# Kernel optimization log

Measured on AMD Instinct MI355X. Metric: run time of the kernel, lower is better.

Reference implementation:

```python
import jax, jax.numpy as jnp
import numpy as np

N, L, H, M, D = 4096, 4096, 8, 64, 64

def setup_inputs() -> dict:
    key = jax.random.key(0)
    kq, kk, kv = jax.random.split(key, 3)
    queries = jax.random.normal(kq, (N, H, M), dtype=jnp.float32)
    keys = jax.random.normal(kk, (L, H, M), dtype=jnp.float32)
    values = jax.random.normal(kv, (L, H, D), dtype=jnp.float32)
    return {"queries": queries, "keys": keys, "values": values}

def reference(queries, keys, values):
    # scores: [n, l, h] = sigmoid(q . k) per head
    attention_num = jax.nn.sigmoid(jnp.einsum('nhm,lhm->nlh', queries, keys))
    # normalizer: sum over l -> [n, h] (torch code broadcasts via wasteful repeat)
    attention_normalizer = jnp.sum(attention_num, axis=1, keepdims=True)  # [n,1,h]
    attention = attention_num / attention_normalizer  # [n,l,h]
    # dropout p=0.0 -> identity
    attn_output = jnp.einsum('nlh,lhd->nhd', attention, values)
    return attn_output
```

## Files before the change

kernel.cpp:

```cpp
#include <hip/hip_runtime.h>
#include <stdint.h>


typedef __bf16 bf16x8 __attribute__((ext_vector_type(8)));
typedef __bf16 bf16x2 __attribute__((ext_vector_type(2)));
typedef float  f32x2  __attribute__((ext_vector_type(2)));
typedef float  f32x16 __attribute__((ext_vector_type(16)));

constexpr int NH = 8, MD = 64, NL = 4096, NN = 4096;
constexpr size_t ONUM_ELEMS = (size_t)NN * NH * MD;
constexpr size_t Z_ELEMS    = (size_t)NN * NH;
constexpr size_t KB_ELEMS   = (size_t)NH * NL * MD;
constexpr size_t VTB_ELEMS  = (size_t)NH * NL * MD;

__device__ __forceinline__ unsigned packbf2(float a, float b) {
  bf16x2 t = __builtin_convertvector((f32x2){a, b}, bf16x2);
  return __builtin_bit_cast(unsigned, t);
}

__device__ __forceinline__ void glds16(const void* g, void* l) {
  __builtin_amdgcn_global_load_lds(
      (const __attribute__((address_space(1))) unsigned int*)g,
      (__attribute__((address_space(3))) unsigned int*)l, 16, 0, 0);
}

__global__ __launch_bounds__(256) void diffattn_prepass(
    const float* __restrict__ Kg, const float* __restrict__ Vg,
    unsigned short* __restrict__ Kb, unsigned short* __restrict__ Vtb) {
  __shared__ __attribute__((aligned(16))) unsigned short Vt_lds[64 * 64];
  const int tid = threadIdx.x;
  const int h = blockIdx.x & 7;
  const int t = blockIdx.x >> 3;

#pragma unroll
  for (int e = 0; e < 2; ++e) {
    const int g = tid * 2 + e;
    const int l = g >> 3, c = g & 7;
    const float* kp = Kg + (((size_t)(t * 64 + l) * NH + h) * MD) + c * 8;
    const float4 a = *(const float4*)kp;
    const float4 b = *(const float4*)(kp + 4);
    unsigned out[4] = {packbf2(a.x, a.y), packbf2(a.z, a.w),
                       packbf2(b.x, b.y), packbf2(b.z, b.w)};
    unsigned short* dst =
        Kb + ((size_t)h * NL + t * 64 + l) * MD + ((c ^ (l & 7)) * 8);
    *(uint4*)dst = *(const uint4*)out;
  }

  {
    const int lr = tid & 63, dbase = (tid >> 6) * 16;
    const float* vp = Vg + (((size_t)(t * 64 + lr) * NH + h) * MD) + dbase;
#pragma unroll
    for (int i = 0; i < 4; ++i) {
      const float4 v = *(const float4*)(vp + i * 4);
      const int d0 = dbase + i * 4;
      Vt_lds[(d0 + 0) * 64 + lr] = __builtin_bit_cast(unsigned short, (__bf16)v.x);
      Vt_lds[(d0 + 1) * 64 + lr] = __builtin_bit_cast(unsigned short, (__bf16)v.y);
      Vt_lds[(d0 + 2) * 64 + lr] = __builtin_bit_cast(unsigned short, (__bf16)v.z);
      Vt_lds[(d0 + 3) * 64 + lr] = __builtin_bit_cast(unsigned short, (__bf16)v.w);
    }
  }
  __syncthreads();
#pragma unroll
  for (int e = 0; e < 2; ++e) {
    const int g = tid * 2 + e;
    const int d = g >> 3, cl = g & 7;
    const uint4 chunk = *(const uint4*)&Vt_lds[d * 64 + cl * 8];
    unsigned short* dst = Vtb + ((size_t)(h * 64 + t) * 64 + d) * 64 +
                          ((cl ^ (d & 7)) * 8);
    *(uint4*)dst = chunk;
  }
}

__global__ __launch_bounds__(256, 4) void diffattn_partial(
    const float* __restrict__ Qg, const unsigned short* __restrict__ Kb,
    const unsigned short* __restrict__ Vtb, float* __restrict__ Onum,
    float* __restrict__ Zp, int nsplit, int lLen) {
  __shared__ __attribute__((aligned(16))) unsigned short Ksh[64 * 64];
  __shared__ __attribute__((aligned(16))) unsigned short Vtsh[64 * 64];

  const int tid  = threadIdx.x;
  const int w    = tid >> 6;
  const int lane = tid & 63;
  const int col  = lane & 31;
  const int hi   = lane >> 5;

  const int h     = blockIdx.x & 7;
  const int tmp   = blockIdx.x >> 3;
  const int split = tmp % nsplit;
  const int n0    = (tmp / nsplit) * 128;
  const int lBeg  = split * lLen;

  bf16x8 qf[4];
  {
    const float* qp = Qg + ((size_t)(n0 + w * 32 + col) * NH + h) * MD;
    const float c = -1.4426950408889634f;
#pragma unroll
    for (int kc = 0; kc < 4; ++kc) {
      const float4 x = *(const float4*)(qp + kc * 16 + hi * 8);
      const float4 y = *(const float4*)(qp + kc * 16 + hi * 8 + 4);
      bf16x8 f;
      f[0] = (__bf16)(c * x.x); f[1] = (__bf16)(c * x.y);
      f[2] = (__bf16)(c * x.z); f[3] = (__bf16)(c * x.w);
      f[4] = (__bf16)(c * y.x); f[5] = (__bf16)(c * y.y);
      f[6] = (__bf16)(c * y.z); f[7] = (__bf16)(c * y.w);
      qf[kc] = f;
    }
  }

  f32x16 oacc[2];
#pragma unroll
  for (int i = 0; i < 16; ++i) { oacc[0][i] = 0.f; oacc[1][i] = 0.f; }
  float zacc = 0.f;

  const char* kgh = (const char*)(Kb + (size_t)h * NL * MD);
  const char* vgh = (const char*)(Vtb + (size_t)h * NL * MD);

  for (int l0 = lBeg; l0 < lBeg + lLen; l0 += 64) {
    const char* kgb = kgh + (size_t)l0 * 128;
    const char* vgb = vgh + (size_t)l0 * 128;
    __syncthreads();
    {
      const int o = w * 2048 + lane * 16;
      glds16(kgb + o,        (char*)Ksh  + w * 2048);
      glds16(kgb + o + 1024, (char*)Ksh  + w * 2048 + 1024);
      glds16(vgb + o,        (char*)Vtsh + w * 2048);
      glds16(vgb + o + 1024, (char*)Vtsh + w * 2048 + 1024);
    }
    __syncthreads();

    f32x16 d1[2];
#pragma unroll
    for (int i = 0; i < 16; ++i) { d1[0][i] = 0.f; d1[1][i] = 0.f; }
#pragma unroll
    for (int lh = 0; lh < 2; ++lh) {
      const int rowK = lh * 32 + col;
      const char* kp = (const char*)Ksh + rowK * 128;
      const int sw = rowK & 7;
#pragma unroll
      for (int kc = 0; kc < 4; ++kc) {
        const bf16x8 kf = *(const bf16x8*)(kp + (((kc << 1) | hi) ^ sw) * 16);
        d1[lh] = __builtin_amdgcn_mfma_f32_32x32x16_bf16(kf, qf[kc], d1[lh], 0, 0, 0);
      }
    }

    unsigned pk[2][8];
#pragma unroll
    for (int lh = 0; lh < 2; ++lh) {
      float s[16];
#pragma unroll
      for (int r = 0; r < 16; ++r) {
        const float e = __builtin_amdgcn_exp2f(d1[lh][r]);
        s[r] = __builtin_amdgcn_rcpf(1.0f + e);
        zacc += s[r];
      }
#pragma unroll
      for (int p = 0; p < 8; ++p) pk[lh][p] = packbf2(s[2 * p], s[2 * p + 1]);
    }

#pragma unroll
    for (int kc2 = 0; kc2 < 4; ++kc2) {
      const int lh = kc2 >> 1, s4 = (kc2 & 1) * 4;
      const unsigned send0 = hi ? pk[lh][s4 + 0] : pk[lh][s4 + 2];
      const unsigned send1 = hi ? pk[lh][s4 + 1] : pk[lh][s4 + 3];
      const unsigned recv0 = (unsigned)__shfl_xor((int)send0, 32, 64);
      const unsigned recv1 = (unsigned)__shfl_xor((int)send1, 32, 64);
      union { unsigned u[4]; bf16x8 v; } pf;
      if (hi == 0) {
        pf.u[0] = pk[lh][s4 + 0]; pf.u[1] = pk[lh][s4 + 1];
        pf.u[2] = recv0;          pf.u[3] = recv1;
      } else {
        pf.u[0] = recv0;          pf.u[1] = recv1;
        pf.u[2] = pk[lh][s4 + 2]; pf.u[3] = pk[lh][s4 + 3];
      }
#pragma unroll
      for (int ds = 0; ds < 2; ++ds) {
        const int rowV = ds * 32 + col;
        const bf16x8 vf = *(const bf16x8*)((const char*)Vtsh + rowV * 128 +
                                           (((kc2 << 1) | hi) ^ (rowV & 7)) * 16);
        oacc[ds] = __builtin_amdgcn_mfma_f32_32x32x16_bf16(pf.v, vf, oacc[ds], 0, 0, 0);
      }
    }
  }

  const float zrow = zacc + __shfl_xor(zacc, 32, 64);
  if (hi == 0)
    Zp[(size_t)split * Z_ELEMS + (size_t)(n0 + w * 32 + col) * NH + h] = zrow;

  float* onum = Onum + (size_t)split * ONUM_ELEMS;
#pragma unroll
  for (int ds = 0; ds < 2; ++ds) {
    const int d = ds * 32 + col;
#pragma unroll
    for (int r = 0; r < 16; ++r) {
      const int row = (r & 3) + 8 * (r >> 2) + 4 * hi;
      onum[((size_t)(n0 + w * 32 + row) * NH + h) * MD + d] = oacc[ds][r];
    }
  }
}

__global__ __launch_bounds__(256) void diffattn_combine(
    const float* __restrict__ Onum, const float* __restrict__ Zp,
    float* __restrict__ Og, int nsplit) {
  const int idx = blockIdx.x * 256 + threadIdx.x;
  if (idx >= (int)(ONUM_ELEMS / 4)) return;
  const int nh = idx >> 4;
  const int d4 = (idx & 15) * 4;
  float z = 0.f;
  float4 o = make_float4(0.f, 0.f, 0.f, 0.f);
  for (int s = 0; s < nsplit; ++s) {
    z += Zp[(size_t)s * Z_ELEMS + nh];
    const float4 t = *(const float4*)(Onum + (size_t)s * ONUM_ELEMS +
                                      (size_t)nh * MD + d4);
    o.x += t.x; o.y += t.y; o.z += t.z; o.w += t.w;
  }
  const float zi = __builtin_amdgcn_rcpf(z);
  float4 r = make_float4(o.x * zi, o.y * zi, o.z * zi, o.w * zi);
  *(float4*)(Og + (size_t)nh * MD + d4) = r;
}

extern "C" void kernel_launch(void* const* d_in, const int* in_sizes, int n_in,
                              void* d_out, int out_size, void* d_ws, size_t ws_size,
                              hipStream_t stream) {
  const float* Q = (const float*)d_in[0];
  const float* K = (const float*)d_in[1];
  const float* V = (const float*)d_in[2];
  float* O = (float*)d_out;

  const size_t conv_bytes = (KB_ELEMS + VTB_ELEMS) * sizeof(unsigned short);
  int nsplit = 4;
  while (nsplit > 1 &&
         (size_t)nsplit * (ONUM_ELEMS + Z_ELEMS) * sizeof(float) + conv_bytes >
             ws_size)
    nsplit >>= 1;

  float* Onum = (float*)d_ws;
  float* Zp   = Onum + (size_t)nsplit * ONUM_ELEMS;
  unsigned short* Kbb = (unsigned short*)(Zp + (size_t)nsplit * Z_ELEMS);
  unsigned short* Vtb = Kbb + KB_ELEMS;

  const int lLen = NL / nsplit;
  diffattn_prepass<<<dim3(8 * (NL / 64)), dim3(256), 0, stream>>>(K, V, Kbb, Vtb);
  diffattn_partial<<<dim3(8 * 32 * nsplit), dim3(256), 0, stream>>>(
      Q, Kbb, Vtb, Onum, Zp, nsplit, lLen);
  diffattn_combine<<<dim3((ONUM_ELEMS / 4 + 255) / 256), dim3(256), 0, stream>>>(
      Onum, Zp, O, nsplit);
}
```

Before: 131.6 us.

## Fuse split-L combine into partial kernel via atomic last-block reduction

Drops the separate combine kernel. Each partial block now increments a per-(n-tile, head) atomic counter, and the last block to finish sums the split partial numerators and normalizers and writes the final output. The split count also rises from 4 to 8 to put more blocks on the GPU. The intent is to save a kernel launch and improve occupancy. In exchange it adds a memset, fences, and a serialized tail reduction in the last block, plus twice the partial-buffer traffic.

```diff
diff --git a/kernel.cpp b/kernel.cpp
--- a/kernel.cpp
+++ b/kernel.cpp
@@ -12,6 +12,7 @@
 constexpr size_t Z_ELEMS    = (size_t)NN * NH;
 constexpr size_t KB_ELEMS   = (size_t)NH * NL * MD;
 constexpr size_t VTB_ELEMS  = (size_t)NH * NL * MD;
+constexpr int NGROUPS = 8 * 32;
 
 __device__ __forceinline__ unsigned packbf2(float a, float b) {
   bf16x2 t = __builtin_convertvector((f32x2){a, b}, bf16x2);
@@ -74,9 +75,12 @@
 __global__ __launch_bounds__(256, 4) void diffattn_partial(
     const float* __restrict__ Qg, const unsigned short* __restrict__ Kb,
     const unsigned short* __restrict__ Vtb, float* __restrict__ Onum,
-    float* __restrict__ Zp, int nsplit, int lLen) {
+    float* __restrict__ Zp, int* __restrict__ cnt, float* __restrict__ Og,
+    int nsplit, int lLen) {
   __shared__ __attribute__((aligned(16))) unsigned short Ksh[64 * 64];
   __shared__ __attribute__((aligned(16))) unsigned short Vtsh[64 * 64];
+  __shared__ float Zred[128];
+  __shared__ int lastSh;
 
   const int tid  = threadIdx.x;
   const int w    = tid >> 6;
@@ -87,7 +91,8 @@
   const int h     = blockIdx.x & 7;
   const int tmp   = blockIdx.x >> 3;
   const int split = tmp % nsplit;
-  const int n0    = (tmp / nsplit) * 128;
+  const int ntile = tmp / nsplit;
+  const int n0    = ntile * 128;
   const int lBeg  = split * lLen;
 
   bf16x8 qf[4];
@@ -196,26 +201,36 @@
       onum[((size_t)(n0 + w * 32 + row) * NH + h) * MD + d] = oacc[ds][r];
     }
   }
-}
-
-__global__ __launch_bounds__(256) void diffattn_combine(
-    const float* __restrict__ Onum, const float* __restrict__ Zp,
-    float* __restrict__ Og, int nsplit) {
-  const int idx = blockIdx.x * 256 + threadIdx.x;
-  if (idx >= (int)(ONUM_ELEMS / 4)) return;
-  const int nh = idx >> 4;
-  const int d4 = (idx & 15) * 4;
-  float z = 0.f;
-  float4 o = make_float4(0.f, 0.f, 0.f, 0.f);
-  for (int s = 0; s < nsplit; ++s) {
-    z += Zp[(size_t)s * Z_ELEMS + nh];
-    const float4 t = *(const float4*)(Onum + (size_t)s * ONUM_ELEMS +
-                                      (size_t)nh * MD + d4);
-    o.x += t.x; o.y += t.y; o.z += t.z; o.w += t.w;
-  }
-  const float zi = __builtin_amdgcn_rcpf(z);
-  float4 r = make_float4(o.x * zi, o.y * zi, o.z * zi, o.w * zi);
-  *(float4*)(Og + (size_t)nh * MD + d4) = r;
+
+  __threadfence();
+  __syncthreads();
+  if (tid == 0) {
+    const int gid = ntile * 8 + h;
+    lastSh = (atomicAdd(&cnt[gid], 1) == nsplit - 1) ? 1 : 0;
+  }
+  __syncthreads();
+  if (!lastSh) return;
+
+  __threadfence();
+  for (int r = tid; r < 128; r += 256) {
+    float z = 0.f;
+    for (int s = 0; s < nsplit; ++s)
+      z += Zp[(size_t)s * Z_ELEMS + (size_t)(n0 + r) * NH + h];
+    Zred[r] = __builtin_amdgcn_rcpf(z);
+  }
+  __syncthreads();
+  for (int j = tid; j < 128 * 16; j += 256) {
+    const int r = j >> 4, c4 = j & 15;
+    const size_t off = ((size_t)(n0 + r) * NH + h) * MD + c4 * 4;
+    float4 acc = make_float4(0.f, 0.f, 0.f, 0.f);
+    for (int s = 0; s < nsplit; ++s) {
+      const float4 t = *(const float4*)(Onum + (size_t)s * ONUM_ELEMS + off);
+      acc.x += t.x; acc.y += t.y; acc.z += t.z; acc.w += t.w;
+    }
+    const float zi = Zred[r];
+    *(float4*)(Og + off) =
+        make_float4(acc.x * zi, acc.y * zi, acc.z * zi, acc.w * zi);
+  }
 }
 
 extern "C" void kernel_launch(void* const* d_in, const int* in_sizes, int n_in,
@@ -226,8 +241,9 @@
   const float* V = (const float*)d_in[2];
   float* O = (float*)d_out;
 
-  const size_t conv_bytes = (KB_ELEMS + VTB_ELEMS) * sizeof(unsigned short);
-  int nsplit = 4;
+  const size_t conv_bytes =
+      (KB_ELEMS + VTB_ELEMS) * sizeof(unsigned short) + NGROUPS * sizeof(int);
+  int nsplit = 8;
   while (nsplit > 1 &&
          (size_t)nsplit * (ONUM_ELEMS + Z_ELEMS) * sizeof(float) + conv_bytes >
              ws_size)
@@ -237,11 +253,11 @@
   float* Zp   = Onum + (size_t)nsplit * ONUM_ELEMS;
   unsigned short* Kbb = (unsigned short*)(Zp + (size_t)nsplit * Z_ELEMS);
   unsigned short* Vtb = Kbb + KB_ELEMS;
-
+  int* cnt = (int*)(Vtb + VTB_ELEMS);
+
+  hipMemsetAsync(cnt, 0, NGROUPS * sizeof(int), stream);
   const int lLen = NL / nsplit;
   diffattn_prepass<<<dim3(8 * (NL / 64)), dim3(256), 0, stream>>>(K, V, Kbb, Vtb);
   diffattn_partial<<<dim3(8 * 32 * nsplit), dim3(256), 0, stream>>>(
-      Q, Kbb, Vtb, Onum, Zp, nsplit, lLen);
-  diffattn_combine<<<dim3((ONUM_ELEMS / 4 + 255) / 256), dim3(256), 0, stream>>>(
-      Onum, Zp, O, nsplit);
-}
+      Q, Kbb, Vtb, Onum, Zp, cnt, O, nsplit, lLen);
+}
```

Result: slower. 441.1 us (+235.2%).

## Double-buffer K/V tiles in LDS to prefetch the next tile during compute

Applied to the files above, without the earlier changes.

The K and V^T tiles in shared memory become two ping-pong buffers. The async global-to-LDS load of tile t+1 is issued right after the barrier, then tile t is computed, leaving one barrier per iteration instead of two. The goal is to hide global-load latency behind the MFMA and sigmoid work. The first MFMA of the score chain now takes a constant zero accumulator instead of zeroing registers. The cost is twice the LDS per block, which could limit how many blocks fit on a CU.

```diff
diff --git a/kernel.cpp b/kernel.cpp
--- a/kernel.cpp
+++ b/kernel.cpp
@@ -75,8 +75,8 @@
     const float* __restrict__ Qg, const unsigned short* __restrict__ Kb,
     const unsigned short* __restrict__ Vtb, float* __restrict__ Onum,
     float* __restrict__ Zp, int nsplit, int lLen) {
-  __shared__ __attribute__((aligned(16))) unsigned short Ksh[64 * 64];
-  __shared__ __attribute__((aligned(16))) unsigned short Vtsh[64 * 64];
+  __shared__ __attribute__((aligned(16))) unsigned short Ksh[2][64 * 64];
+  __shared__ __attribute__((aligned(16))) unsigned short Vtsh[2][64 * 64];
 
   const int tid  = threadIdx.x;
   const int w    = tid >> 6;
@@ -111,33 +111,46 @@
 #pragma unroll
   for (int i = 0; i < 16; ++i) { oacc[0][i] = 0.f; oacc[1][i] = 0.f; }
   float zacc = 0.f;
+  const f32x16 zf = {};
 
   const char* kgh = (const char*)(Kb + (size_t)h * NL * MD);
   const char* vgh = (const char*)(Vtb + (size_t)h * NL * MD);
-
-  for (int l0 = lBeg; l0 < lBeg + lLen; l0 += 64) {
-    const char* kgb = kgh + (size_t)l0 * 128;
-    const char* vgb = vgh + (size_t)l0 * 128;
+  const int o = w * 2048 + lane * 16;
+  const int T = lLen >> 6;
+
+  {
+    const char* kgb = kgh + (size_t)lBeg * 128;
+    const char* vgb = vgh + (size_t)lBeg * 128;
+    glds16(kgb + o,        (char*)Ksh[0]  + w * 2048);
+    glds16(kgb + o + 1024, (char*)Ksh[0]  + w * 2048 + 1024);
+    glds16(vgb + o,        (char*)Vtsh[0] + w * 2048);
+    glds16(vgb + o + 1024, (char*)Vtsh[0] + w * 2048 + 1024);
+  }
+
+  for (int t = 0; t < T; ++t) {
+    const int cur = t & 1;
     __syncthreads();
-    {
-      const int o = w * 2048 + lane * 16;
-      glds16(kgb + o,        (char*)Ksh  + w * 2048);
-      glds16(kgb + o + 1024, (char*)Ksh  + w * 2048 + 1024);
-      glds16(vgb + o,        (char*)Vtsh + w * 2048);
-      glds16(vgb + o + 1024, (char*)Vtsh + w * 2048 + 1024);
-    }
-    __syncthreads();
+    if (t + 1 < T) {
+      const char* kgb = kgh + (size_t)(lBeg + (t + 1) * 64) * 128;
+      const char* vgb = vgh + (size_t)(lBeg + (t + 1) * 64) * 128;
+      glds16(kgb + o,        (char*)Ksh[cur ^ 1]  + w * 2048);
+      glds16(kgb + o + 1024, (char*)Ksh[cur ^ 1]  + w * 2048 + 1024);
+      glds16(vgb + o,        (char*)Vtsh[cur ^ 1] + w * 2048);
+      glds16(vgb + o + 1024, (char*)Vtsh[cur ^ 1] + w * 2048 + 1024);
+    }
 
     f32x16 d1[2];
-#pragma unroll
-    for (int i = 0; i < 16; ++i) { d1[0][i] = 0.f; d1[1][i] = 0.f; }
 #pragma unroll
     for (int lh = 0; lh < 2; ++lh) {
       const int rowK = lh * 32 + col;
-      const char* kp = (const char*)Ksh + rowK * 128;
+      const char* kp = (const char*)Ksh[cur] + rowK * 128;
       const int sw = rowK & 7;
-#pragma unroll
-      for (int kc = 0; kc < 4; ++kc) {
+      {
+        const bf16x8 kf = *(const bf16x8*)(kp + ((hi ^ sw) * 16));
+        d1[lh] = __builtin_amdgcn_mfma_f32_32x32x16_bf16(kf, qf[0], zf, 0, 0, 0);
+      }
+#pragma unroll
+      for (int kc = 1; kc < 4; ++kc) {
         const bf16x8 kf = *(const bf16x8*)(kp + (((kc << 1) | hi) ^ sw) * 16);
         d1[lh] = __builtin_amdgcn_mfma_f32_32x32x16_bf16(kf, qf[kc], d1[lh], 0, 0, 0);
       }
@@ -175,8 +188,9 @@
 #pragma unroll
       for (int ds = 0; ds < 2; ++ds) {
         const int rowV = ds * 32 + col;
-        const bf16x8 vf = *(const bf16x8*)((const char*)Vtsh + rowV * 128 +
-                                           (((kc2 << 1) | hi) ^ (rowV & 7)) * 16);
+        const bf16x8 vf =
+            *(const bf16x8*)((const char*)Vtsh[cur] + rowV * 128 +
+                             (((kc2 << 1) | hi) ^ (rowV & 7)) * 16);
         oacc[ds] = __builtin_amdgcn_mfma_f32_32x32x16_bf16(pf.v, vf, oacc[ds], 0, 0, 0);
       }
     }
```

New measurement: 132.0 us. No clear change (+0.3%).

## Load K and V fragments directly from global memory, dropping LDS staging

Applied to the files above, without the earlier changes.

Removes the shared-memory staging of K and transposed V tiles and the two barriers per tile. Each wave now reads its bf16 MFMA fragments straight from global memory (through the caches), using precomputed swizzled offsets, and prefetches V fragments in two halves. This removes the LDS round trip and block-wide synchronisation. In exchange, all four waves re-read the same K/V data from L1/L2 and global-load latency is exposed inside the loop without explicit double buffering.

```diff
diff --git a/kernel.cpp b/kernel.cpp
--- a/kernel.cpp
+++ b/kernel.cpp
@@ -16,12 +16,6 @@
 __device__ __forceinline__ unsigned packbf2(float a, float b) {
   bf16x2 t = __builtin_convertvector((f32x2){a, b}, bf16x2);
   return __builtin_bit_cast(unsigned, t);
-}
-
-__device__ __forceinline__ void glds16(const void* g, void* l) {
-  __builtin_amdgcn_global_load_lds(
-      (const __attribute__((address_space(1))) unsigned int*)g,
-      (__attribute__((address_space(3))) unsigned int*)l, 16, 0, 0);
 }
 
 __global__ __launch_bounds__(256) void diffattn_prepass(
@@ -75,9 +69,6 @@
     const float* __restrict__ Qg, const unsigned short* __restrict__ Kb,
     const unsigned short* __restrict__ Vtb, float* __restrict__ Onum,
     float* __restrict__ Zp, int nsplit, int lLen) {
-  __shared__ __attribute__((aligned(16))) unsigned short Ksh[64 * 64];
-  __shared__ __attribute__((aligned(16))) unsigned short Vtsh[64 * 64];
-
   const int tid  = threadIdx.x;
   const int w    = tid >> 6;
   const int lane = tid & 63;
@@ -111,37 +102,40 @@
 #pragma unroll
   for (int i = 0; i < 16; ++i) { oacc[0][i] = 0.f; oacc[1][i] = 0.f; }
   float zacc = 0.f;
-
-  const char* kgh = (const char*)(Kb + (size_t)h * NL * MD);
-  const char* vgh = (const char*)(Vtb + (size_t)h * NL * MD);
-
-  for (int l0 = lBeg; l0 < lBeg + lLen; l0 += 64) {
-    const char* kgb = kgh + (size_t)l0 * 128;
-    const char* vgb = vgh + (size_t)l0 * 128;
-    __syncthreads();
-    {
-      const int o = w * 2048 + lane * 16;
-      glds16(kgb + o,        (char*)Ksh  + w * 2048);
-      glds16(kgb + o + 1024, (char*)Ksh  + w * 2048 + 1024);
-      glds16(vgb + o,        (char*)Vtsh + w * 2048);
-      glds16(vgb + o + 1024, (char*)Vtsh + w * 2048 + 1024);
-    }
-    __syncthreads();
-
+  const f32x16 zf = {};
+
+  const int sw = col & 7;
+  int off[2][4];
+#pragma unroll
+  for (int a = 0; a < 2; ++a)
+#pragma unroll
+    for (int c = 0; c < 4; ++c)
+      off[a][c] = a * 4096 + col * 128 + ((((c << 1) | hi) ^ sw) * 16);
+
+  const char* kgb = (const char*)(Kb + (size_t)h * NL * MD) + (size_t)lBeg * 128;
+  const char* vgb = (const char*)(Vtb + (size_t)h * NL * MD) + (size_t)lBeg * 128;
+  const int T = lLen >> 6;
+
+  for (int t = 0; t < T; ++t) {
     f32x16 d1[2];
 #pragma unroll
-    for (int i = 0; i < 16; ++i) { d1[0][i] = 0.f; d1[1][i] = 0.f; }
-#pragma unroll
     for (int lh = 0; lh < 2; ++lh) {
-      const int rowK = lh * 32 + col;
-      const char* kp = (const char*)Ksh + rowK * 128;
-      const int sw = rowK & 7;
-#pragma unroll
-      for (int kc = 0; kc < 4; ++kc) {
-        const bf16x8 kf = *(const bf16x8*)(kp + (((kc << 1) | hi) ^ sw) * 16);
-        d1[lh] = __builtin_amdgcn_mfma_f32_32x32x16_bf16(kf, qf[kc], d1[lh], 0, 0, 0);
-      }
-    }
+      const bf16x8 kf0 = *(const bf16x8*)(kgb + off[lh][0]);
+      const bf16x8 kf1 = *(const bf16x8*)(kgb + off[lh][1]);
+      const bf16x8 kf2 = *(const bf16x8*)(kgb + off[lh][2]);
+      const bf16x8 kf3 = *(const bf16x8*)(kgb + off[lh][3]);
+      d1[lh] = __builtin_amdgcn_mfma_f32_32x32x16_bf16(kf0, qf[0], zf, 0, 0, 0);
+      d1[lh] = __builtin_amdgcn_mfma_f32_32x32x16_bf16(kf1, qf[1], d1[lh], 0, 0, 0);
+      d1[lh] = __builtin_amdgcn_mfma_f32_32x32x16_bf16(kf2, qf[2], d1[lh], 0, 0, 0);
+      d1[lh] = __builtin_amdgcn_mfma_f32_32x32x16_bf16(kf3, qf[3], d1[lh], 0, 0, 0);
+    }
+
+    bf16x8 vf[2][2];
+#pragma unroll
+    for (int kc2 = 0; kc2 < 2; ++kc2)
+#pragma unroll
+      for (int ds = 0; ds < 2; ++ds)
+        vf[kc2][ds] = *(const bf16x8*)(vgb + off[ds][kc2]);
 
     unsigned pk[2][8];
 #pragma unroll
@@ -159,6 +153,13 @@
 
 #pragma unroll
     for (int kc2 = 0; kc2 < 4; ++kc2) {
+      if (kc2 == 2) {
+#pragma unroll
+        for (int k2 = 2; k2 < 4; ++k2)
+#pragma unroll
+          for (int ds = 0; ds < 2; ++ds)
+            vf[k2 - 2][ds] = *(const bf16x8*)(vgb + off[ds][k2]);
+      }
       const int lh = kc2 >> 1, s4 = (kc2 & 1) * 4;
       const unsigned send0 = hi ? pk[lh][s4 + 0] : pk[lh][s4 + 2];
       const unsigned send1 = hi ? pk[lh][s4 + 1] : pk[lh][s4 + 3];
@@ -174,12 +175,12 @@
       }
 #pragma unroll
       for (int ds = 0; ds < 2; ++ds) {
-        const int rowV = ds * 32 + col;
-        const bf16x8 vf = *(const bf16x8*)((const char*)Vtsh + rowV * 128 +
-                                           (((kc2 << 1) | hi) ^ (rowV & 7)) * 16);
-        oacc[ds] = __builtin_amdgcn_mfma_f32_32x32x16_bf16(pf.v, vf, oacc[ds], 0, 0, 0);
-      }
-    }
+        oacc[ds] = __builtin_amdgcn_mfma_f32_32x32x16_bf16(
+            pf.v, vf[kc2 & 1][ds], oacc[ds], 0, 0, 0);
+      }
+    }
+    kgb += 8192;
+    vgb += 8192;
   }
 
   const float zrow = zacc + __shfl_xor(zacc, 32, 64);
```

Result: slower. 176.4 us (+34.0%).
